# Performance work log

Hardware: AMD Instinct MI355X
Metric: run time of the kernel (lower is better)

The kernel has to match this reference:

```python
import jax, jax.numpy as jnp
import numpy as np

N_ROUNDS = 8
BUCKET = 64          # chunk_dim
MAX_LEN = 4096
HIDDEN = 128
MAX_N_ROUNDS = 16
N_HASHES = MAX_LEN // BUCKET  # 64
BATCH = 8


def setup_inputs() -> dict:
    key = jax.random.key(0)
    x = jax.random.normal(key, (BATCH, MAX_LEN, HIDDEN), dtype=jnp.float32)
    # random_matrix buffer: stack of top-n_hashes rows of QR(Q) of gaussian matrices
    rng = np.random.default_rng(0)
    mats = []
    for _ in range(MAX_N_ROUNDS):
        q, _ = np.linalg.qr(rng.standard_normal((HIDDEN, HIDDEN)).astype(np.float64))
        mats.append(q[:N_HASHES])
    random_matrix = jnp.asarray(np.stack(mats), dtype=jnp.float32)  # (16, 64, 128)
    return {"x": x, "random_matrix": random_matrix}


def reference(x, random_matrix):
    # Faithful translation of AngularLocalSensitiveHashing.return_sorted
    # (perm over rounds taken as identity; pad_dim == 0 since max_len % bucket == 0).
    b, l, d = x.shape
    r = N_ROUNDS
    xr = jnp.broadcast_to(x, (r, b, l, d))                      # (r,b,l,d)
    # F.normalize(x, dim=-1) with eps=1e-12
    xn = xr / jnp.maximum(jnp.linalg.norm(xr, axis=-1, keepdims=True), 1e-12)
    rm = random_matrix[:r]                                      # (r,c,d)
    rot = jnp.einsum('rbld,rcd->rblc', xn, rm)                  # (r,b,l,c)
    # angular LSH bucket id in [1, 2c]
    hashes = jnp.argmax(jnp.concatenate([rot, -rot], axis=3), axis=3) + 1  # (r,b,l) int
    positions = jnp.arange(l)
    sort_keys = hashes * l + positions                          # bucket-major, position-stable
    sorted_indices = jnp.argsort(sort_keys, axis=2, stable=True)  # (r,b,l)
    x_sorted = jnp.take_along_axis(xr, sorted_indices[..., None], axis=2)  # (r,b,l,d)
    x_sorted = x_sorted.reshape(r, b, l // BUCKET, BUCKET, d)
    sorted_hashes = jnp.sort(hashes, axis=2).reshape(r, b, l // BUCKET, BUCKET)
    return x_sorted, sorted_hashes, sorted_indices[..., None]
```

## Files before the change

kernel.cpp:

```cpp
#include <hip/hip_runtime.h>
#include <stdint.h>

#define R_ 8
#define B_ 8
#define L_ 4096
#define D_ 128
#define C_ 64
#define ROWS_BL 32768
#define XS_ELEMS 33554432
#define HS_ELEMS 262144

__global__ __launch_bounds__(256) void khash(const float* __restrict__ x,
                                             const float* __restrict__ rm,
                                             uint16_t* __restrict__ hws) {
    int row = blockIdx.x * 256 + threadIdx.x;
    int r = blockIdx.y;
    const float* xr = x + (size_t)row * D_;

    double s = 0.0;
    double n0 = 0.0, n1 = 0.0, n2 = 0.0, n3 = 0.0;
#pragma unroll
    for (int d = 0; d < D_; d += 4) {
        double v0 = (double)xr[d+0], v1 = (double)xr[d+1];
        double v2 = (double)xr[d+2], v3 = (double)xr[d+3];
        n0 = fma(v0, v0, n0); n1 = fma(v1, v1, n1);
        n2 = fma(v2, v2, n2); n3 = fma(v3, v3, n3);
    }
    s = (n0 + n1) + (n2 + n3);
    double norm = sqrt(s);
    if (norm < 1e-12) norm = 1e-12;
    double rinv = 1.0 / norm;

    const float* w = rm + (size_t)r * (C_ * D_);
    double acc[C_];
#pragma unroll
    for (int c = 0; c < C_; ++c) acc[c] = 0.0;

    for (int chunk = 0; chunk < 4; ++chunk) {
        double q[32];
        const float* xc = xr + chunk * 32;
#pragma unroll
        for (int j = 0; j < 32; ++j) q[j] = (double)xc[j] * rinv;
        const float* wc0 = w + chunk * 32;
        for (int c = 0; c < C_; ++c) {
            const float* wc = wc0 + c * D_;
            double a0 = 0.0, a1 = 0.0, a2 = 0.0, a3 = 0.0;
#pragma unroll
            for (int j = 0; j < 32; j += 4) {
                a0 = fma(q[j+0], (double)wc[j+0], a0);
                a1 = fma(q[j+1], (double)wc[j+1], a1);
                a2 = fma(q[j+2], (double)wc[j+2], a2);
                a3 = fma(q[j+3], (double)wc[j+3], a3);
            }
            acc[c] += ((a0 + a1) + (a2 + a3));
        }
    }

    double bp = -1e300, bn = -1e300;
    int bpi = 0, bni = 0;
#pragma unroll
    for (int c = 0; c < C_; ++c) {
        double v = acc[c];
        if (v > bp) { bp = v; bpi = c; }
        if (-v > bn) { bn = -v; bni = c; }
    }
    int idx = (bp >= bn) ? bpi : (C_ + bni);
    hws[((size_t)r << 15) + row] = (uint16_t)idx;
}

__global__ __launch_bounds__(256) void ksort(uint16_t* __restrict__ hws,
                                             float* __restrict__ out) {
    int rb = blockIdx.x;
    int t = threadIdx.x;
    __shared__ uint16_t h[4096];
    __shared__ uint16_t cnt[64 * 128];
    __shared__ uint16_t inv[4096];
    __shared__ int base[128];
    uint16_t* slice = hws + ((size_t)rb << 12);
    for (int i = t; i < 4096; i += 256) h[i] = slice[i];
    for (int i = t; i < 8192; i += 256) cnt[i] = 0;
    __syncthreads();
    if (t < 64) {
        uint16_t* c = cnt + (t << 7);
        const uint16_t* hh = h + (t << 6);
        for (int i = 0; i < 64; ++i) c[hh[i] & 127]++;
    }
    __syncthreads();
    if (t < 128) {
        int run = 0;
        for (int ch = 0; ch < 64; ++ch) {
            int v = cnt[(ch << 7) + t];
            cnt[(ch << 7) + t] = (uint16_t)run;
            run += v;
        }
        base[t] = run;
    }
    __syncthreads();
    if (t == 0) {
        int run = 0;
        for (int bin = 0; bin < 128; ++bin) { int v = base[bin]; base[bin] = run; run += v; }
    }
    __syncthreads();
    if (t < 64) {
        uint16_t* c = cnt + (t << 7);
        const uint16_t* hh = h + (t << 6);
        int p0 = t << 6;
        for (int i = 0; i < 64; ++i) {
            int bin = hh[i] & 127;
            int dest = base[bin] + c[bin];
            c[bin]++;
            inv[dest] = (uint16_t)(p0 + i);
        }
    }
    __syncthreads();
    float* out_h = out + XS_ELEMS;
    float* out_i = out + XS_ELEMS + HS_ELEMS;
    int obase = rb << 12;
    for (int dst = t; dst < 4096; dst += 256) {
        int p = inv[dst];
        out_h[obase + dst] = (float)((h[p] & 127) + 1);
        out_i[obase + dst] = (float)p;
        slice[dst] = (uint16_t)p;
    }
}

__global__ void kgather(const float* __restrict__ x,
                        const uint16_t* __restrict__ inv,
                        float4* __restrict__ outx) {
    int id = blockIdx.x * 256 + threadIdx.x;
    int lane = id & 31;
    int rowg = id >> 5;
    int b = (rowg >> 12) & 7;
    int src = inv[rowg] & 4095;
    const float4* xp = (const float4*)x;
    outx[id] = xp[((size_t)((b << 12) + src) << 5) + lane];
}

extern "C" void kernel_launch(void* const* d_in, const int* in_sizes, int n_in,
                              void* d_out, int out_size, void* d_ws, size_t ws_size,
                              hipStream_t stream) {
    const float* x  = (const float*)d_in[0];
    const float* rm = (const float*)d_in[1];
    float* out = (float*)d_out;
    uint16_t* hws = (uint16_t*)d_ws;

    khash<<<dim3(ROWS_BL / 256, R_), 256, 0, stream>>>(x, rm, hws);
    ksort<<<dim3(R_ * B_), 256, 0, stream>>>(hws, out);
    kgather<<<dim3((XS_ELEMS / 4) / 256), 256, 0, stream>>>(x, hws, (float4*)out);
}
```

Baseline: 550.5 us.

## Compute LSH projections in fp32 with fp64 fallback on near-ties

The hash kernel now loads each row into registers as float4 and computes the 64 projections in fp32, tracking the top two values of the concatenated [rot, -rot] vector. Only when the margin between the best and second-best is under a small threshold does it recompute the argmax in fp64. The aim is to avoid the slow double-precision FMA path for most rows while keeping the argmax matching the reference. The threshold is a heuristic error bound on fp32 accumulation, so a wrong hash is possible if the fp32 error exceeds it. Holding 128 floats per thread also raises register pressure.

```diff
diff --git a/kernel.cpp b/kernel.cpp
--- a/kernel.cpp
+++ b/kernel.cpp
@@ -15,56 +15,70 @@
                                              uint16_t* __restrict__ hws) {
     int row = blockIdx.x * 256 + threadIdx.x;
     int r = blockIdx.y;
-    const float* xr = x + (size_t)row * D_;
 
-    double s = 0.0;
+    float xv[128];
+    const float4* xp = (const float4*)(x + (size_t)row * D_);
+#pragma unroll
+    for (int k = 0; k < 32; ++k) {
+        float4 v = xp[k];
+        xv[4*k+0] = v.x; xv[4*k+1] = v.y; xv[4*k+2] = v.z; xv[4*k+3] = v.w;
+    }
+
     double n0 = 0.0, n1 = 0.0, n2 = 0.0, n3 = 0.0;
 #pragma unroll
     for (int d = 0; d < D_; d += 4) {
-        double v0 = (double)xr[d+0], v1 = (double)xr[d+1];
-        double v2 = (double)xr[d+2], v3 = (double)xr[d+3];
+        double v0 = (double)xv[d+0], v1 = (double)xv[d+1];
+        double v2 = (double)xv[d+2], v3 = (double)xv[d+3];
         n0 = fma(v0, v0, n0); n1 = fma(v1, v1, n1);
         n2 = fma(v2, v2, n2); n3 = fma(v3, v3, n3);
     }
-    s = (n0 + n1) + (n2 + n3);
-    double norm = sqrt(s);
+    double norm = sqrt((n0 + n1) + (n2 + n3));
     if (norm < 1e-12) norm = 1e-12;
     double rinv = 1.0 / norm;
+    float rinvf = (float)rinv;
 
     const float* w = rm + (size_t)r * (C_ * D_);
-    double acc[C_];
+
+    float m1 = -__builtin_inff(), m2 = -__builtin_inff();
+    int i1 = 0;
+    for (int c = 0; c < C_; ++c) {
+        const float* wc = w + (c << 7);
+        float a0 = 0.f, a1 = 0.f, a2 = 0.f, a3 = 0.f;
 #pragma unroll
-    for (int c = 0; c < C_; ++c) acc[c] = 0.0;
+        for (int j = 0; j < 128; j += 4) {
+            a0 = fmaf(xv[j+0], wc[j+0], a0);
+            a1 = fmaf(xv[j+1], wc[j+1], a1);
+            a2 = fmaf(xv[j+2], wc[j+2], a2);
+            a3 = fmaf(xv[j+3], wc[j+3], a3);
+        }
+        float rot = ((a0 + a1) + (a2 + a3)) * rinvf;
+        if (rot > m1)      { m2 = m1; m1 = rot; i1 = c; }
+        else if (rot > m2) { m2 = rot; }
+        float nr = -rot;
+        if (nr > m1)       { m2 = m1; m1 = nr; i1 = C_ + c; }
+        else if (nr > m2)  { m2 = nr; }
+    }
 
-    for (int chunk = 0; chunk < 4; ++chunk) {
-        double q[32];
-        const float* xc = xr + chunk * 32;
-#pragma unroll
-        for (int j = 0; j < 32; ++j) q[j] = (double)xc[j] * rinv;
-        const float* wc0 = w + chunk * 32;
+    int idx = i1;
+    if (!(m1 - m2 >= 4e-5f)) {
+        double bp = -1e300, bn = -1e300;
+        int bpi = 0, bni = 0;
         for (int c = 0; c < C_; ++c) {
-            const float* wc = wc0 + c * D_;
+            const float* wc = w + (c << 7);
             double a0 = 0.0, a1 = 0.0, a2 = 0.0, a3 = 0.0;
 #pragma unroll
-            for (int j = 0; j < 32; j += 4) {
-                a0 = fma(q[j+0], (double)wc[j+0], a0);
-                a1 = fma(q[j+1], (double)wc[j+1], a1);
-                a2 = fma(q[j+2], (double)wc[j+2], a2);
-                a3 = fma(q[j+3], (double)wc[j+3], a3);
+            for (int j = 0; j < 128; j += 4) {
+                a0 = fma((double)xv[j+0] * rinv, (double)wc[j+0], a0);
+                a1 = fma((double)xv[j+1] * rinv, (double)wc[j+1], a1);
+                a2 = fma((double)xv[j+2] * rinv, (double)wc[j+2], a2);
+                a3 = fma((double)xv[j+3] * rinv, (double)wc[j+3], a3);
             }
-            acc[c] += ((a0 + a1) + (a2 + a3));
+            double v = (a0 + a1) + (a2 + a3);
+            if (v > bp)  { bp = v;  bpi = c; }
+            if (-v > bn) { bn = -v; bni = c; }
         }
+        idx = (bp >= bn) ? bpi : (C_ + bni);
     }
-
-    double bp = -1e300, bn = -1e300;
-    int bpi = 0, bni = 0;
-#pragma unroll
-    for (int c = 0; c < C_; ++c) {
-        double v = acc[c];
-        if (v > bp) { bp = v; bpi = c; }
-        if (-v > bn) { bn = -v; bni = c; }
-    }
-    int idx = (bp >= bn) ? bpi : (C_ + bni);
     hws[((size_t)r << 15) + row] = (uint16_t)idx;
 }
 
```

Result: slower. 710.1 us (+29.0%).
